# Performance work log

Measured on AMD Instinct MI355X. Metric: run time of the kernel, lower is better.

Reference implementation:

```python
import jax, jax.numpy as jnp
import numpy as np

B, C, H, W = 2, 256, 64, 64
N_HEAD = 4
GROUPS = 32
EPS = 1e-5


def setup_inputs() -> dict:
    key = jax.random.key(0)
    ks = jax.random.split(key, 6)
    x = jax.random.normal(ks[0], (B, C, H, W), dtype=jnp.float32)
    # GroupNorm affine (perturbed from torch default 1/0 so grads are nontrivial)
    gn_scale = 1.0 + 0.02 * jax.random.normal(ks[1], (C,), dtype=jnp.float32)
    gn_bias = 0.02 * jax.random.normal(ks[2], (C,), dtype=jnp.float32)
    # 1x1 convs == pointwise matmuls: qkv (bias=False), out (bias=True)
    w_qkv = 0.02 * jax.random.normal(ks[3], (3 * C, C), dtype=jnp.float32)
    w_out = 0.02 * jax.random.normal(ks[4], (C, C), dtype=jnp.float32)
    b_out = 0.02 * jax.random.normal(ks[5], (C,), dtype=jnp.float32)
    return {"x": x, "gn_scale": gn_scale, "gn_bias": gn_bias,
            "w_qkv": w_qkv, "w_out": w_out, "b_out": b_out}


def _group_norm(x, scale, bias):
    b, c, h, w = x.shape
    xr = x.reshape(b, GROUPS, c // GROUPS, h, w)
    mean = jnp.mean(xr, axis=(2, 3, 4), keepdims=True)
    var = jnp.var(xr, axis=(2, 3, 4), keepdims=True)
    xr = (xr - mean) * jax.lax.rsqrt(var + EPS)
    x = xr.reshape(b, c, h, w)
    return x * scale[None, :, None, None] + bias[None, :, None, None]


def reference(x, gn_scale, gn_bias, w_qkv, w_out, b_out):
    b, c, h, w = x.shape
    head_dim = c // N_HEAD
    n = h * w
    norm = _group_norm(x, gn_scale, gn_bias)
    # 1x1 conv -> pointwise channel matmul; flatten spatial to n = h*w tokens
    qkv = jnp.einsum('oc,bcn->bon', w_qkv, norm.reshape(b, c, n))
    qkv = qkv.reshape(b, N_HEAD, 3 * head_dim, n)
    q, k, v = jnp.split(qkv, 3, axis=2)  # each [b, n_head, head_dim, n]
    # NOTE: original scales by sqrt(channel), not sqrt(head_dim)
    attn = jnp.einsum('bndq,bndk->bnqk', q, k) / jnp.sqrt(jnp.float32(c))
    attn = jax.nn.softmax(attn, axis=-1)  # [b, n_head, n, n]
    out = jnp.einsum('bnqk,bndk->bndq', attn, v)  # [b, n_head, head_dim, n]
    out = out.reshape(b, c, n)
    out = jnp.einsum('oc,bcn->bon', w_out, out) + b_out[None, :, None]
    return out.reshape(b, c, h, w) + x
```

## Files before the change

kernel.cpp:

```cpp
#include <hip/hip_runtime.h>
#include <hip/hip_bf16.h>

#define Bz 2
#define Cc 256
#define Nn 4096
#define NH 4
#define HD 64
#define NG 32
#define CPG 8
#define EPSv 1e-5f
#define NSPLIT 4
#define GNPART 4

typedef __bf16 bf16x8 __attribute__((ext_vector_type(8)));
typedef __bf16 bf16x4 __attribute__((ext_vector_type(4)));
typedef float f32x4 __attribute__((ext_vector_type(4)));
using bf16_t = __hip_bfloat16;

#define MFMA(a, b, c) __builtin_amdgcn_mfma_f32_16x16x32_bf16(a, b, c, 0, 0, 0)

#define GLOAD_LDS(g, l)                                                        \
  __builtin_amdgcn_global_load_lds(                                            \
      (const __attribute__((address_space(1))) void*)(g),                      \
      (__attribute__((address_space(3))) void*)(l), 16, 0, 0)

#define EXP2(x)                                                                \
  ({ float _r, _x = (x); asm("v_exp_f32 %0, %1" : "=v"(_r) : "v"(_x)); _r; })

#define MAX3F(a, b, c)                                                         \
  ({ float _m; asm("v_max3_f32 %0, %1, %2, %3"                                 \
                   : "=v"(_m) : "v"(a), "v"(b), "v"(c)); _m; })

__device__ __forceinline__ bf16x8 ldb8(const bf16_t* p) {
  return *reinterpret_cast<const bf16x8*>(p);
}

__global__ __launch_bounds__(256) void gn_reduce(const float* __restrict__ x,
                                                 float* __restrict__ stats4) {
  int bg = blockIdx.x;
  int part = blockIdx.y;
  const float4* p4 = reinterpret_cast<const float4*>(
      x + (size_t)bg * (CPG * Nn) + (size_t)part * (CPG * Nn / GNPART));
  float s = 0.f, ss = 0.f;
  for (int i = threadIdx.x; i < CPG * Nn / GNPART / 4; i += 256) {
    float4 v = p4[i];
    s += v.x + v.y + v.z + v.w;
    ss += v.x * v.x + v.y * v.y + v.z * v.z + v.w * v.w;
  }
#pragma unroll
  for (int off = 32; off > 0; off >>= 1) {
    s += __shfl_down(s, off);
    ss += __shfl_down(ss, off);
  }
  __shared__ float ps[4], pss[4];
  int wid = threadIdx.x >> 6;
  if ((threadIdx.x & 63) == 0) { ps[wid] = s; pss[wid] = ss; }
  __syncthreads();
  if (threadIdx.x == 0) {
    stats4[(bg * GNPART + part) * 2] = ps[0] + ps[1] + ps[2] + ps[3];
    stats4[(bg * GNPART + part) * 2 + 1] = pss[0] + pss[1] + pss[2] + pss[3];
  }
}

__global__ __launch_bounds__(256) void gn_apply(const float* __restrict__ x,
    const float* __restrict__ stats4, const float* __restrict__ sc,
    const float* __restrict__ bi, bf16_t* __restrict__ normt) {
  int b = blockIdx.z, c0 = blockIdx.y * 64, n0 = blockIdx.x * 64;
  __shared__ __align__(16) __bf16 t[64][72];
  int cx = threadIdx.x & 15, cy0 = threadIdx.x >> 4;
  const float inv = 1.f / (float)(CPG * Nn);
#pragma unroll
  for (int j = 0; j < 4; j++) {
    int c = c0 + cy0 + j * 16;
    int bg = b * NG + (c >> 3);
    float S = stats4[bg * 8] + stats4[bg * 8 + 2] + stats4[bg * 8 + 4] + stats4[bg * 8 + 6];
    float SS = stats4[bg * 8 + 1] + stats4[bg * 8 + 3] + stats4[bg * 8 + 5] + stats4[bg * 8 + 7];
    float mean = S * inv;
    float rstd = rsqrtf(SS * inv - mean * mean + EPSv);
    float a = rstd * sc[c];
    float bb = bi[c] - mean * a;
    float4 v = *reinterpret_cast<const float4*>(x + ((size_t)b * Cc + c) * Nn + n0 + cx * 4);
    bf16x4 w;
    w[0] = (__bf16)(v.x * a + bb); w[1] = (__bf16)(v.y * a + bb);
    w[2] = (__bf16)(v.z * a + bb); w[3] = (__bf16)(v.w * a + bb);
    *reinterpret_cast<bf16x4*>(&t[cy0 + j * 16][cx * 4]) = w;
  }
  __syncthreads();
  int ny = threadIdx.x >> 2, ch0 = threadIdx.x & 3;
#pragma unroll
  for (int j = 0; j < 2; j++) {
    int ch = ch0 + j * 4;
    bf16x8 o;
#pragma unroll
    for (int jj = 0; jj < 8; jj++) o[jj] = t[ch * 8 + jj][ny];
    *reinterpret_cast<bf16x8*>(normt + ((size_t)b * Nn + n0 + ny) * Cc + c0 + ch * 8) = o;
  }
}

__global__ __launch_bounds__(256) void conv_w(const float* __restrict__ wq,
    const float* __restrict__ wo, bf16_t* __restrict__ wqb,
    bf16_t* __restrict__ wob) {
  int i = blockIdx.x * 256 + threadIdx.x;
  if (i < 768 * Cc) wqb[i] = __float2bfloat16(wq[i]);
  if (i < Cc * Cc) wob[i] = __float2bfloat16(wo[i]);
}

__global__ __launch_bounds__(512) void qkv_gemm(const bf16_t* __restrict__ normt,
    const bf16_t* __restrict__ w, bf16_t* __restrict__ Qt,
    bf16_t* __restrict__ Kt, bf16_t* __restrict__ V) {
  int b = blockIdx.z;
  int h = blockIdx.y;
  int n0 = blockIdx.x * 128;
  int tid = threadIdx.x;
  int wid = tid >> 6, lane = tid & 63;
  int lr = lane & 15, lk = lane >> 4;

  __shared__ __align__(16) bf16_t wbuf[64 * 256];
  __shared__ __align__(16) __bf16 tt[128 * 80];

  const bf16_t* an = normt + ((size_t)b * Nn + n0 + wid * 16 + lr) * Cc + lk * 8;
  bf16x8 a[8];
#pragma unroll
  for (int kk = 0; kk < 8; kk++) a[kk] = ldb8(an + kk * 32);

#pragma unroll
  for (int part = 0; part < 3; part++) {
    int o0 = h * 192 + part * 64;
#pragma unroll
    for (int rnd = 0; rnd < 4; rnd++) {
      int u = rnd * 512 + tid;
      int row = u >> 5, cu = u & 31;
      int cus = (cu & 24) | ((cu & 7) ^ (row & 7));
      GLOAD_LDS(w + (size_t)(o0 + row) * Cc + cus * 8, &wbuf[u * 8]);
    }
    __syncthreads();
    f32x4 acc[4] = {};
#pragma unroll
    for (int kk = 0; kk < 8; kk++)
#pragma unroll
      for (int os = 0; os < 4; os++) {
        bf16x8 bb = ldb8(&wbuf[(os * 16 + lr) * Cc + (((kk * 4 + lk) ^ (lr & 7)) * 8)]);
        acc[os] = MFMA(a[kk], bb, acc[os]);
      }
#pragma unroll
    for (int os = 0; os < 4; os++)
#pragma unroll
      for (int r = 0; r < 4; r++)
        tt[(wid * 16 + lk * 4 + r) * 80 + os * 16 + lr] = (__bf16)acc[os][r];
    __syncthreads();
    if (part < 2) {
      bf16_t* dst = (part == 0 ? Qt : Kt) + (size_t)(b * NH + h) * Nn * HD + (size_t)n0 * HD;
      int n = tid >> 2, dch = (tid & 3) * 16;
      bf16x8 o1 = ldb8(reinterpret_cast<const bf16_t*>(&tt[n * 80 + dch]));
      bf16x8 o2 = ldb8(reinterpret_cast<const bf16_t*>(&tt[n * 80 + dch + 8]));
      *reinterpret_cast<bf16x8*>(dst + (size_t)n * HD + dch) = o1;
      *reinterpret_cast<bf16x8*>(dst + (size_t)n * HD + dch + 8) = o2;
    } else {
      bf16_t* dst = V + (size_t)(b * NH + h) * HD * Nn + n0;
      int d = tid >> 3, nch = (tid & 7) * 16;
      bf16x8 o1, o2;
#pragma unroll
      for (int j = 0; j < 8; j++) {
        o1[j] = tt[(nch + j) * 80 + d];
        o2[j] = tt[(nch + 8 + j) * 80 + d];
      }
      *reinterpret_cast<bf16x8*>(dst + (size_t)d * Nn + nch) = o1;
      *reinterpret_cast<bf16x8*>(dst + (size_t)d * Nn + nch + 8) = o2;
    }
  }
}

__global__ __launch_bounds__(512, 4) void attn_kern(const bf16_t* __restrict__ Qt,
    const bf16_t* __restrict__ Kt, const bf16_t* __restrict__ V,
    bf16_t* __restrict__ Opart, float* __restrict__ ml) {
  int z = blockIdx.z;
  int b = z & 1, sp = z >> 1;
  int h = blockIdx.y;
  int wid = threadIdx.x >> 6, lane = threadIdx.x & 63;
  int lr = lane & 15, lk = lane >> 4;
  int q0 = blockIdx.x * 128 + wid * 16;
  size_t bh = (size_t)(b * NH + h);
  const bf16_t* qp = Qt + (bh * Nn + q0 + lr) * HD + lk * 8;
  bf16x8 aq0 = ldb8(qp), aq1 = ldb8(qp + 32);
  const bf16_t* kglob = Kt + bh * Nn * HD;
  const bf16_t* vglob = V + bh * HD * Nn;
  int kbeg = sp * (Nn / NSPLIT);

  __shared__ __align__(16) char lds[51200];

  int su = (wid & 3) * 64 + lane;
  int srow = su >> 3, scc = su & 7;
  int swz = (scc ^ (srow & 7)) * 8;
  const bf16_t* ksrc = kglob + (size_t)(kbeg + srow) * HD + swz;
  const bf16_t* vsrc = vglob + (size_t)srow * Nn + kbeg + swz;

  int x0 = lr & 7;
  int aK = lr * 128 + ((lk ^ x0) * 16);
  int aK1 = aK ^ 64;
  int pwo = 32768 + wid * 2304 + lr * 144 + lk * 8;
  int pro = 32768 + wid * 2304 + lr * 144 + lk * 16;

  f32x4 acc[4] = {};
  f32x4 lacc = {};
  float m_r = -1e30f;
  const float lam = 0.0625f * 1.44269504088896f;
  const int NT = (Nn / NSPLIT) / 64;

#define LD8(off) (*reinterpret_cast<const bf16x8*>(lds + (off)))

#define STAGE(buf, t)                                                          \
  do {                                                                         \
    if (wid < 4) {                                                             \
      GLOAD_LDS(ksrc + (size_t)(t) * 64 * HD,                                  \
                lds + (buf) * 8192 + (wid & 3) * 1024);                        \
      GLOAD_LDS(ksrc + (size_t)(t) * 64 * HD + 32 * HD,                        \
                lds + (buf) * 8192 + (wid & 3) * 1024 + 4096);                 \
    } else {                                                                   \
      GLOAD_LDS(vsrc + (size_t)(t) * 64,                                       \
                lds + 16384 + (buf) * 8192 + (wid & 3) * 1024);                \
      GLOAD_LDS(vsrc + (size_t)(t) * 64 + (size_t)32 * Nn,                     \
                lds + 16384 + (buf) * 8192 + (wid & 3) * 1024 + 4096);         \
    }                                                                          \
  } while (0)

#define STEP(t, buf)                                                           \
  do {                                                                         \
    __syncthreads();                                                           \
    STAGE(buf ^ 1, (t) + 1);                                                   \
    f32x4 s0 = {}, s1 = {}, s2 = {}, s3 = {};                                  \
    __builtin_amdgcn_s_setprio(1);                                             \
    s0 = MFMA(LD8(aK + (buf) * 8192), aq0, s0);                                \
    s0 = MFMA(LD8(aK1 + (buf) * 8192), aq1, s0);                               \
    s1 = MFMA(LD8(aK + (buf) * 8192 + 2048), aq0, s1);                         \
    s1 = MFMA(LD8(aK1 + (buf) * 8192 + 2048), aq1, s1);                        \
    s2 = MFMA(LD8(aK + (buf) * 8192 + 4096), aq0, s2);                         \
    s2 = MFMA(LD8(aK1 + (buf) * 8192 + 4096), aq1, s2);                        \
    s3 = MFMA(LD8(aK + (buf) * 8192 + 6144), aq0, s3);                         \
    s3 = MFMA(LD8(aK1 + (buf) * 8192 + 6144), aq1, s3);                        \
    __builtin_amdgcn_s_setprio(0);                                             \
    float _t0 = MAX3F(s0[0], s0[1], s0[2]);                                    \
    float _t1 = MAX3F(s0[3], s1[0], s1[1]);                                    \
    float _t2 = MAX3F(s1[2], s1[3], s2[0]);                                    \
    float _t3 = MAX3F(s2[1], s2[2], s2[3]);                                    \
    float _t4 = MAX3F(s3[0], s3[1], s3[2]);                                    \
    float pm = fmaxf(MAX3F(_t0, _t1, _t2), MAX3F(_t3, _t4, s3[3]));            \
    if (!__all(pm <= m_r + 64.f)) {      \
      float pmw = fmaxf(pm, __shfl_xor(pm, 16));                               \
      pmw = fmaxf(pmw, __shfl_xor(pmw, 32));                                   \
      float mn = fmaxf(m_r, pmw);                                              \
      float sf = EXP2((m_r - mn) * lam);                                       \
      m_r = mn;                                                                \
      lacc = lacc * sf;                                                        \
      acc[0] = acc[0] * sf; acc[1] = acc[1] * sf;                              \
      acc[2] = acc[2] * sf; acc[3] = acc[3] * sf;                              \
    }                                                                          \
    float mnl = m_r * lam;                                                     \
    f32x4 p0, p1, p2, p3;                                                      \
    _Pragma("unroll") for (int r = 0; r < 4; r++) {                            \
      p0[r] = EXP2(s0[r] * lam - mnl);                                         \
      p1[r] = EXP2(s1[r] * lam - mnl);                                         \
      p2[r] = EXP2(s2[r] * lam - mnl);                                         \
      p3[r] = EXP2(s3[r] * lam - mnl);                                         \
    }                                                                          \
    lacc += (p0 + p1) + (p2 + p3);                                             \
    bf16x4 w0, w1, w2, w3;                                                     \
    _Pragma("unroll") for (int r = 0; r < 4; r++) {                            \
      w0[r] = (__bf16)p0[r]; w1[r] = (__bf16)p1[r];                            \
      w2[r] = (__bf16)p2[r]; w3[r] = (__bf16)p3[r];                            \
    }                                                                          \
    *reinterpret_cast<bf16x4*>(lds + pwo) = w0;                                \
    *reinterpret_cast<bf16x4*>(lds + pwo + 32) = w1;                           \
    *reinterpret_cast<bf16x4*>(lds + pwo + 64) = w2;                           \
    *reinterpret_cast<bf16x4*>(lds + pwo + 96) = w3;                           \
    bf16x8 pa0 = LD8(pro);                                                     \
    bf16x8 pa1 = LD8(pro + 64);                                                \
    __builtin_amdgcn_s_setprio(1);                                             \
    acc[0] = MFMA(LD8(aK + 16384 + (buf) * 8192), pa0, acc[0]);                \
    acc[0] = MFMA(LD8(aK1 + 16384 + (buf) * 8192), pa1, acc[0]);               \
    acc[1] = MFMA(LD8(aK + 16384 + (buf) * 8192 + 2048), pa0, acc[1]);         \
    acc[1] = MFMA(LD8(aK1 + 16384 + (buf) * 8192 + 2048), pa1, acc[1]);        \
    acc[2] = MFMA(LD8(aK + 16384 + (buf) * 8192 + 4096), pa0, acc[2]);         \
    acc[2] = MFMA(LD8(aK1 + 16384 + (buf) * 8192 + 4096), pa1, acc[2]);        \
    acc[3] = MFMA(LD8(aK + 16384 + (buf) * 8192 + 6144), pa0, acc[3]);         \
    acc[3] = MFMA(LD8(aK1 + 16384 + (buf) * 8192 + 6144), pa1, acc[3]);        \
    __builtin_amdgcn_s_setprio(0);                                             \
  } while (0)

  STAGE(0, 0);
  for (int t = 0; t < NT; t += 2) {
    STEP(t, 0);
    STEP(t + 1, 1);
  }
#undef STEP
#undef STAGE
#undef LD8

  float l_r = (lacc[0] + lacc[1]) + (lacc[2] + lacc[3]);
  l_r += __shfl_xor(l_r, 16);
  l_r += __shfl_xor(l_r, 32);
  float inv_l = 1.f / l_r;
  bf16_t* obase = Opart + (((size_t)z * NH + h) * Nn + q0 + lr) * HD + lk * 4;
#pragma unroll
  for (int dt = 0; dt < 4; dt++) {
    bf16x4 ov;
#pragma unroll
    for (int r = 0; r < 4; r++) ov[r] = (__bf16)(acc[dt][r] * inv_l);
    *reinterpret_cast<bf16x4*>(obase + dt * 16) = ov;
  }
  if (lk == 0) {
    float2 mlv = make_float2(m_r, l_r);
    *reinterpret_cast<float2*>(ml + (((size_t)z * NH + h) * Nn + q0 + lr) * 2) = mlv;
  }
}

__global__ __launch_bounds__(256) void attn_merge(const bf16_t* __restrict__ Opart,
    const float* __restrict__ ml, bf16_t* __restrict__ At) {
  int gid = blockIdx.x * 256 + threadIdx.x;
  int d0 = (gid & 7) * 8;
  int q = (gid >> 3) & (Nn - 1);
  int h = (gid >> 15) & (NH - 1);
  int b = gid >> 17;
  const float lam = 0.0625f * 1.44269504088896f;
  size_t zi[NSPLIT];
  float mv[NSPLIT], lv[NSPLIT], wv[NSPLIT];
  float M = -1e30f;
#pragma unroll
  for (int s = 0; s < NSPLIT; s++) {
    zi[s] = ((size_t)(s * Bz + b) * NH + h) * Nn + q;
    mv[s] = ml[zi[s] * 2];
    lv[s] = ml[zi[s] * 2 + 1];
    M = fmaxf(M, mv[s]);
  }
  float L = 0.f;
#pragma unroll
  for (int s = 0; s < NSPLIT; s++) {
    wv[s] = lv[s] * EXP2((mv[s] - M) * lam);
    L += wv[s];
  }
  float invL = 1.f / L;
  float o[8] = {};
#pragma unroll
  for (int s = 0; s < NSPLIT; s++) {
    bf16x8 a = ldb8(Opart + zi[s] * HD + d0);
#pragma unroll
    for (int r = 0; r < 8; r++) o[r] += (float)a[r] * wv[s];
  }
  bf16x8 ov;
#pragma unroll
  for (int r = 0; r < 8; r++) ov[r] = (__bf16)(o[r] * invL);
  *reinterpret_cast<bf16x8*>(At + ((size_t)b * Nn + q) * Cc + h * HD + d0) = ov;
}

__global__ __launch_bounds__(256) void out_gemm(const bf16_t* __restrict__ At,
    const bf16_t* __restrict__ w, const float* __restrict__ bo,
    const float* __restrict__ x, float* __restrict__ out) {
  int b = blockIdx.z;
  int o0 = blockIdx.y * 64;
  int n0 = blockIdx.x * 64;
  int tid = threadIdx.x;
  int wid = tid >> 6;
  int lane = tid & 63;
  int lr = lane & 15, lk = lane >> 4;

  __shared__ __align__(16) char smem[64 * 256 * 2];
  bf16_t* wbuf = (bf16_t*)smem;
  float(*t)[68] = (float(*)[68])smem;

#pragma unroll
  for (int rnd = 0; rnd < 8; rnd++) {
    int u = rnd * 256 + tid;
    int row = u >> 5, cu = u & 31;
    int cus = (cu & 24) | ((cu & 7) ^ (row & 7));
    GLOAD_LDS(w + (size_t)(o0 + row) * Cc + cus * 8, &wbuf[u * 8]);
  }
  const bf16_t* aa = At + ((size_t)b * Nn + n0 + wid * 16 + lr) * Cc + lk * 8;
  f32x4 acc[4] = {};
  __syncthreads();
#pragma unroll
  for (int kk = 0; kk < Cc / 32; kk++) {
    bf16x8 a = ldb8(aa + kk * 32);
#pragma unroll
    for (int os = 0; os < 4; os++) {
      bf16x8 bb = ldb8(&wbuf[(os * 16 + lr) * Cc + (((kk * 4 + lk) ^ (lr & 7)) * 8)]);
      acc[os] = MFMA(a, bb, acc[os]);
    }
  }
  __syncthreads();
#pragma unroll
  for (int os = 0; os < 4; os++)
#pragma unroll
    for (int r = 0; r < 4; r++)
      t[wid * 16 + lk * 4 + r][os * 16 + lr] = acc[os][r];
  __syncthreads();
  int orow = tid >> 2;
  int nch = (tid & 3) * 16;
  size_t base = ((size_t)b * Cc + o0 + orow) * Nn + n0 + nch;
  float bv = bo[o0 + orow];
#pragma unroll
  for (int j = 0; j < 16; j++)
    out[base + j] = t[nch + j][orow] + bv + x[base + j];
}

extern "C" void kernel_launch(void* const* d_in, const int* in_sizes, int n_in,
                              void* d_out, int out_size, void* d_ws, size_t ws_size,
                              hipStream_t stream) {
  const float* x = (const float*)d_in[0];
  const float* gn_scale = (const float*)d_in[1];
  const float* gn_bias = (const float*)d_in[2];
  const float* w_qkv = (const float*)d_in[3];
  const float* w_out = (const float*)d_in[4];
  const float* b_out = (const float*)d_in[5];
  float* out = (float*)d_out;
  char* ws = (char*)d_ws;

  float* stats4 = (float*)(ws + 0);
  bf16_t* wout_b = (bf16_t*)(ws + 4096);
  bf16_t* Qt = (bf16_t*)(ws + 139264);
  bf16_t* At = (bf16_t*)(ws + 139264);
  bf16_t* Kt = (bf16_t*)(ws + 4333568);
  bf16_t* V = (bf16_t*)(ws + 8527872);
  bf16_t* wqkv_b = (bf16_t*)(ws + 12722176);
  bf16_t* normt = (bf16_t*)(ws + 13115392);
  bf16_t* Opart = (bf16_t*)(ws + 12722176);
  float* ml = (float*)(ws + 29499392);

  conv_w<<<768, 256, 0, stream>>>(w_qkv, w_out, wqkv_b, wout_b);
  gn_reduce<<<dim3(Bz * NG, GNPART), 256, 0, stream>>>(x, stats4);
  gn_apply<<<dim3(Nn / 64, Cc / 64, Bz), 256, 0, stream>>>(x, stats4, gn_scale, gn_bias, normt);
  qkv_gemm<<<dim3(Nn / 128, NH, Bz), 512, 0, stream>>>(normt, wqkv_b, Qt, Kt, V);
  attn_kern<<<dim3(Nn / 128, NH, Bz * NSPLIT), 512, 0, stream>>>(Qt, Kt, V, Opart, ml);
  attn_merge<<<Bz * NH * Nn * HD / 8 / 256, 256, 0, stream>>>(Opart, ml, At);
  out_gemm<<<dim3(Nn / 64, Cc / 64, Bz), 256, 0, stream>>>(At, wout_b, b_out, x, out);
}
```

Baseline: 89.29 us.

## Prescale Q by softmax factor and stage K/V through registers into padded LDS

Q is multiplied by the scale·log2e factor once at load time, so the per-element multiply in the exp2 argument and the rescale factor disappear, and the split merge drops its lam multiply. K/V tiles are now fetched into registers and written to padded (144-byte-stride) LDS rows with one buffer and two barriers per tile, replacing the double-buffered direct global-to-LDS loads with XOR swizzle. The LDS footprint shrinks and the launch-bounds target rises to 8 waves per SIMD, which trades register budget for occupancy. The lazy-rescale threshold is tightened to match the new log2 units. Rounding Q to bf16 after scaling adds some precision loss.

```diff
diff --git a/kernel.cpp b/kernel.cpp
--- a/kernel.cpp
+++ b/kernel.cpp
@@ -170,73 +170,60 @@
   }
 }
 
-__global__ __launch_bounds__(512, 4) void attn_kern(const bf16_t* __restrict__ Qt,
+__global__ __launch_bounds__(512, 8) void attn_kern(const bf16_t* __restrict__ Qt,
     const bf16_t* __restrict__ Kt, const bf16_t* __restrict__ V,
     bf16_t* __restrict__ Opart, float* __restrict__ ml) {
   int z = blockIdx.z;
   int b = z & 1, sp = z >> 1;
   int h = blockIdx.y;
-  int wid = threadIdx.x >> 6, lane = threadIdx.x & 63;
+  int tid = threadIdx.x;
+  int wid = tid >> 6, lane = tid & 63;
   int lr = lane & 15, lk = lane >> 4;
   int q0 = blockIdx.x * 128 + wid * 16;
   size_t bh = (size_t)(b * NH + h);
+  const float lam = 0.0625f * 1.44269504088896f;
+
   const bf16_t* qp = Qt + (bh * Nn + q0 + lr) * HD + lk * 8;
-  bf16x8 aq0 = ldb8(qp), aq1 = ldb8(qp + 32);
-  const bf16_t* kglob = Kt + bh * Nn * HD;
-  const bf16_t* vglob = V + bh * HD * Nn;
+  bf16x8 q0v = ldb8(qp), q1v = ldb8(qp + 32);
+  bf16x8 aq0, aq1;
+#pragma unroll
+  for (int j = 0; j < 8; j++) {
+    aq0[j] = (__bf16)((float)q0v[j] * lam);
+    aq1[j] = (__bf16)((float)q1v[j] * lam);
+  }
   int kbeg = sp * (Nn / NSPLIT);
 
-  __shared__ __align__(16) char lds[51200];
-
-  int su = (wid & 3) * 64 + lane;
-  int srow = su >> 3, scc = su & 7;
-  int swz = (scc ^ (srow & 7)) * 8;
-  const bf16_t* ksrc = kglob + (size_t)(kbeg + srow) * HD + swz;
-  const bf16_t* vsrc = vglob + (size_t)srow * Nn + kbeg + swz;
-
-  int x0 = lr & 7;
-  int aK = lr * 128 + ((lk ^ x0) * 16);
-  int aK1 = aK ^ 64;
-  int pwo = 32768 + wid * 2304 + lr * 144 + lk * 8;
-  int pro = 32768 + wid * 2304 + lr * 144 + lk * 16;
+  __shared__ __align__(16) char lds[36864];
+
+  int srow = tid >> 3, scu = tid & 7;
+  const bf16_t* kg = Kt + bh * Nn * HD + (size_t)(kbeg + srow) * HD + scu * 8;
+  const bf16_t* vg = V + bh * HD * Nn + (size_t)srow * Nn + kbeg + scu * 8;
+  char* kw = lds + srow * 144 + scu * 16;
+  char* vw = lds + 9216 + srow * 144 + scu * 16;
+
+  int aK = lr * 144 + lk * 16;
+  int pwo = 18432 + wid * 2304 + lr * 144 + lk * 8;
+  int pro = 18432 + wid * 2304 + lr * 144 + lk * 16;
 
   f32x4 acc[4] = {};
   f32x4 lacc = {};
   float m_r = -1e30f;
-  const float lam = 0.0625f * 1.44269504088896f;
   const int NT = (Nn / NSPLIT) / 64;
 
 #define LD8(off) (*reinterpret_cast<const bf16x8*>(lds + (off)))
 
-#define STAGE(buf, t)                                                          \
+#define STEP_COMPUTE                                                           \
   do {                                                                         \
-    if (wid < 4) {                                                             \
-      GLOAD_LDS(ksrc + (size_t)(t) * 64 * HD,                                  \
-                lds + (buf) * 8192 + (wid & 3) * 1024);                        \
-      GLOAD_LDS(ksrc + (size_t)(t) * 64 * HD + 32 * HD,                        \
-                lds + (buf) * 8192 + (wid & 3) * 1024 + 4096);                 \
-    } else {                                                                   \
-      GLOAD_LDS(vsrc + (size_t)(t) * 64,                                       \
-                lds + 16384 + (buf) * 8192 + (wid & 3) * 1024);                \
-      GLOAD_LDS(vsrc + (size_t)(t) * 64 + (size_t)32 * Nn,                     \
-                lds + 16384 + (buf) * 8192 + (wid & 3) * 1024 + 4096);         \
-    }                                                                          \
-  } while (0)
-
-#define STEP(t, buf)                                                           \
-  do {                                                                         \
-    __syncthreads();                                                           \
-    STAGE(buf ^ 1, (t) + 1);                                                   \
     f32x4 s0 = {}, s1 = {}, s2 = {}, s3 = {};                                  \
     __builtin_amdgcn_s_setprio(1);                                             \
-    s0 = MFMA(LD8(aK + (buf) * 8192), aq0, s0);                                \
-    s0 = MFMA(LD8(aK1 + (buf) * 8192), aq1, s0);                               \
-    s1 = MFMA(LD8(aK + (buf) * 8192 + 2048), aq0, s1);                         \
-    s1 = MFMA(LD8(aK1 + (buf) * 8192 + 2048), aq1, s1);                        \
-    s2 = MFMA(LD8(aK + (buf) * 8192 + 4096), aq0, s2);                         \
-    s2 = MFMA(LD8(aK1 + (buf) * 8192 + 4096), aq1, s2);                        \
-    s3 = MFMA(LD8(aK + (buf) * 8192 + 6144), aq0, s3);                         \
-    s3 = MFMA(LD8(aK1 + (buf) * 8192 + 6144), aq1, s3);                        \
+    s0 = MFMA(LD8(aK), aq0, s0);                                               \
+    s0 = MFMA(LD8(aK + 64), aq1, s0);                                          \
+    s1 = MFMA(LD8(aK + 2304), aq0, s1);                                        \
+    s1 = MFMA(LD8(aK + 2368), aq1, s1);                                        \
+    s2 = MFMA(LD8(aK + 4608), aq0, s2);                                        \
+    s2 = MFMA(LD8(aK + 4672), aq1, s2);                                        \
+    s3 = MFMA(LD8(aK + 6912), aq0, s3);                                        \
+    s3 = MFMA(LD8(aK + 6976), aq1, s3);                                        \
     __builtin_amdgcn_s_setprio(0);                                             \
     float _t0 = MAX3F(s0[0], s0[1], s0[2]);                                    \
     float _t1 = MAX3F(s0[3], s1[0], s1[1]);                                    \
@@ -244,23 +231,22 @@
     float _t3 = MAX3F(s2[1], s2[2], s2[3]);                                    \
     float _t4 = MAX3F(s3[0], s3[1], s3[2]);                                    \
     float pm = fmaxf(MAX3F(_t0, _t1, _t2), MAX3F(_t3, _t4, s3[3]));            \
-    if (!__all(pm <= m_r + 64.f)) {      \
+    if (!__all(pm <= m_r + 4.f)) {       \
       float pmw = fmaxf(pm, __shfl_xor(pm, 16));                               \
       pmw = fmaxf(pmw, __shfl_xor(pmw, 32));                                   \
       float mn = fmaxf(m_r, pmw);                                              \
-      float sf = EXP2((m_r - mn) * lam);                                       \
+      float sf = EXP2(m_r - mn);                                               \
       m_r = mn;                                                                \
       lacc = lacc * sf;                                                        \
       acc[0] = acc[0] * sf; acc[1] = acc[1] * sf;                              \
       acc[2] = acc[2] * sf; acc[3] = acc[3] * sf;                              \
     }                                                                          \
-    float mnl = m_r * lam;                                                     \
     f32x4 p0, p1, p2, p3;                                                      \
     _Pragma("unroll") for (int r = 0; r < 4; r++) {                            \
-      p0[r] = EXP2(s0[r] * lam - mnl);                                         \
-      p1[r] = EXP2(s1[r] * lam - mnl);                                         \
-      p2[r] = EXP2(s2[r] * lam - mnl);                                         \
-      p3[r] = EXP2(s3[r] * lam - mnl);                                         \
+      p0[r] = EXP2(s0[r] - m_r);                                               \
+      p1[r] = EXP2(s1[r] - m_r);                                               \
+      p2[r] = EXP2(s2[r] - m_r);                                               \
+      p3[r] = EXP2(s3[r] - m_r);                                               \
     }                                                                          \
     lacc += (p0 + p1) + (p2 + p3);                                             \
     bf16x4 w0, w1, w2, w3;                                                     \
@@ -275,24 +261,37 @@
     bf16x8 pa0 = LD8(pro);                                                     \
     bf16x8 pa1 = LD8(pro + 64);                                                \
     __builtin_amdgcn_s_setprio(1);                                             \
-    acc[0] = MFMA(LD8(aK + 16384 + (buf) * 8192), pa0, acc[0]);                \
-    acc[0] = MFMA(LD8(aK1 + 16384 + (buf) * 8192), pa1, acc[0]);               \
-    acc[1] = MFMA(LD8(aK + 16384 + (buf) * 8192 + 2048), pa0, acc[1]);         \
-    acc[1] = MFMA(LD8(aK1 + 16384 + (buf) * 8192 + 2048), pa1, acc[1]);        \
-    acc[2] = MFMA(LD8(aK + 16384 + (buf) * 8192 + 4096), pa0, acc[2]);         \
-    acc[2] = MFMA(LD8(aK1 + 16384 + (buf) * 8192 + 4096), pa1, acc[2]);        \
-    acc[3] = MFMA(LD8(aK + 16384 + (buf) * 8192 + 6144), pa0, acc[3]);         \
-    acc[3] = MFMA(LD8(aK1 + 16384 + (buf) * 8192 + 6144), pa1, acc[3]);        \
+    acc[0] = MFMA(LD8(aK + 9216), pa0, acc[0]);                                \
+    acc[0] = MFMA(LD8(aK + 9280), pa1, acc[0]);                                \
+    acc[1] = MFMA(LD8(aK + 11520), pa0, acc[1]);                               \
+    acc[1] = MFMA(LD8(aK + 11584), pa1, acc[1]);                               \
+    acc[2] = MFMA(LD8(aK + 13824), pa0, acc[2]);                               \
+    acc[2] = MFMA(LD8(aK + 13888), pa1, acc[2]);                               \
+    acc[3] = MFMA(LD8(aK + 16128), pa0, acc[3]);                               \
+    acc[3] = MFMA(LD8(aK + 16192), pa1, acc[3]);                               \
     __builtin_amdgcn_s_setprio(0);                                             \
   } while (0)
 
-  STAGE(0, 0);
-  for (int t = 0; t < NT; t += 2) {
-    STEP(t, 0);
-    STEP(t + 1, 1);
-  }
-#undef STEP
-#undef STAGE
+  bf16x8 kreg = ldb8(kg);
+  bf16x8 vreg = ldb8(vg);
+  *reinterpret_cast<bf16x8*>(kw) = kreg;
+  *reinterpret_cast<bf16x8*>(vw) = vreg;
+  __syncthreads();
+
+  for (int t = 0; t < NT; t++) {
+    if (t + 1 < NT) {
+      kreg = ldb8(kg + (size_t)(t + 1) * 64 * HD);
+      vreg = ldb8(vg + (t + 1) * 64);
+    }
+    STEP_COMPUTE;
+    if (t + 1 < NT) {
+      __syncthreads();
+      *reinterpret_cast<bf16x8*>(kw) = kreg;
+      *reinterpret_cast<bf16x8*>(vw) = vreg;
+      __syncthreads();
+    }
+  }
+#undef STEP_COMPUTE
 #undef LD8
 
   float l_r = (lacc[0] + lacc[1]) + (lacc[2] + lacc[3]);
@@ -320,7 +319,6 @@
   int q = (gid >> 3) & (Nn - 1);
   int h = (gid >> 15) & (NH - 1);
   int b = gid >> 17;
-  const float lam = 0.0625f * 1.44269504088896f;
   size_t zi[NSPLIT];
   float mv[NSPLIT], lv[NSPLIT], wv[NSPLIT];
   float M = -1e30f;
@@ -334,7 +332,7 @@
   float L = 0.f;
 #pragma unroll
   for (int s = 0; s < NSPLIT; s++) {
-    wv[s] = lv[s] * EXP2((mv[s] - M) * lam);
+    wv[s] = lv[s] * EXP2(mv[s] - M);
     L += wv[s];
   }
   float invL = 1.f / L;
```

Result: slower. 117.0 us (+31.1%).
